# Optimization experiments

Hardware: AMD Instinct MI355X
Metric: run time of the kernel (lower is better)

## Reference

```python
import jax, jax.numpy as jnp
import numpy as np

N = 8256        # 32 graphs * 258 nodes (view in gencoder_mine requires multiple of 258)
E = 132096      # avg degree 16
D = 32          # encoding_size (in = out node feats of NNConv)
HALF = D // 2
HID = 128
NG = 32         # number of graphs
PER = 258       # hard-coded nodes per graph
OUT = 128       # out_feats
EPS = 1e-5


def _lrelu(x):
    return jnp.where(x >= 0, x, 0.2 * x)


def setup_inputs() -> dict:
    key = jax.random.key(0)
    ks = jax.random.split(key, 24)
    rn = lambda i, shape, s=0.05: jax.random.normal(ks[i], shape, dtype=jnp.float32) * s
    return {
        "pos": jax.random.normal(ks[0], (N, 3), dtype=jnp.float32),
        "vel": jax.random.normal(ks[1], (N, 3), dtype=jnp.float32),
        "edge_idx": jax.random.randint(ks[2], (2, E), 0, N),
        # node / velocity encoders: Linear(3,128) -> LeakyReLU(0.2) -> Linear(128, D/2)
        "ne_w1": rn(3, (3, HID)), "ne_b1": jnp.zeros((HID,), jnp.float32),
        "ne_w2": rn(4, (HID, HALF)), "ne_b2": jnp.zeros((HALF,), jnp.float32),
        "ve_w1": rn(5, (3, HID)), "ve_b1": jnp.zeros((HID,), jnp.float32),
        "ve_w2": rn(6, (HID, HALF)), "ve_b2": jnp.zeros((HALF,), jnp.float32),
        # edge_func: MLP(1, D*D): Lin(1,128)-ReLU-Lin(128,128)-ReLU-Lin(128,D*D) (SHARED by both conv layers)
        "em_w1": rn(7, (1, HID)), "em_b1": jnp.zeros((HID,), jnp.float32),
        "em_w2": rn(8, (HID, HID)), "em_b2": jnp.zeros((HID,), jnp.float32),
        "em_w3": rn(9, (HID, D * D), 0.02), "em_b3": jnp.zeros((D * D,), jnp.float32),
        "conv_b": jnp.zeros((D,), jnp.float32),  # shared NNConv bias
        # per-layer BatchNorm1d affine params
        "bn1_g": jnp.ones((D,), jnp.float32), "bn1_b": jnp.zeros((D,), jnp.float32),
        "bn2_g": jnp.ones((D,), jnp.float32), "bn2_b": jnp.zeros((D,), jnp.float32),
        # final LayerNorm(D)
        "ln_g": jnp.ones((D,), jnp.float32), "ln_b": jnp.zeros((D,), jnp.float32),
        # MLPbig_to_small: Lin(258*D,128)-LeakyReLU-Lin(128,OUT)
        "fc_w1": rn(10, (PER * D, HID)), "fc_b1": jnp.zeros((HID,), jnp.float32),
        "fc_w2": rn(11, (HID, OUT)), "fc_b2": jnp.zeros((OUT,), jnp.float32),
    }


def reference(pos, vel, edge_idx, ne_w1, ne_b1, ne_w2, ne_b2, ve_w1, ve_b1, ve_w2, ve_b2,
              em_w1, em_b1, em_w2, em_b2, em_w3, em_b3, conv_b,
              bn1_g, bn1_b, bn2_g, bn2_b, ln_g, ln_b, fc_w1, fc_b1, fc_w2, fc_b2):
    center = edge_idx[0]   # edge dst (messages flow neigh -> center)
    neigh = edge_idx[1]    # edge src

    # cosine-cutoff edge weight: 1/2 * (cos(dist*pi/max(dist)) + 1)
    diff = pos[center] - pos[neigh]                      # [E,3]
    dist = jnp.sqrt(jnp.sum(diff * diff, axis=1))        # [E]
    w = 0.5 * (jnp.cos(dist * jnp.pi / jnp.max(dist)) + 1.0)

    # node features: concat of pos/vel encoders -> [N, D]
    h = jnp.concatenate([
        _lrelu(pos @ ne_w1 + ne_b1) @ ne_w2 + ne_b2,
        _lrelu(vel @ ve_w1 + ve_b1) @ ve_w2 + ve_b2,
    ], axis=1)

    # per-edge NNConv weight matrices (edge MLP is shared across both conv layers)
    z = jax.nn.relu(w[:, None] @ em_w1 + em_b1)
    z = jax.nn.relu(z @ em_w2 + em_b2)
    We = (z @ em_w3 + em_b3).reshape(E, D, D)            # [E, D, D]

    deg = jax.ops.segment_sum(jnp.ones((E,), h.dtype), center, num_segments=N)
    denom = jnp.maximum(deg, 1.0)[:, None]

    # two conv layers: h = NNConv(BatchNorm(h)) + h  (shared NNConv weights)
    for g, b in ((bn1_g, bn1_b), (bn2_g, bn2_b)):
        mu = h.mean(axis=0)
        var = h.var(axis=0)  # biased, as in torch BN training mode
        hn = (h - mu) * jax.lax.rsqrt(var + EPS) * g + b
        msg = jnp.einsum('ed,edf->ef', hn[neigh], We)    # gather + per-edge matmul
        agg = jax.ops.segment_sum(msg, center, num_segments=N) / denom  # mean scatter
        h = agg + conv_b + h

    # LayerNorm over feature dim
    mu = h.mean(axis=-1, keepdims=True)
    var = h.var(axis=-1, keepdims=True)
    h = (h - mu) * jax.lax.rsqrt(var + EPS) * ln_g + ln_b

    # reshape to [NG, 258*D] and decode
    out = h.reshape(NG, PER * D)
    out = _lrelu(out @ fc_w1 + fc_b1) @ fc_w2 + fc_b2    # [NG, OUT]
    return out
```

## Files before the change

### kernel.cpp

```cpp
#include <hip/hip_runtime.h>
#include <hip/hip_bf16.h>

#define NNODE 8256
#define NEDGE 132096
#define DD 32
#define HIDN 128
#define NGR 32
#define PERG 258
#define KPG (PERG*DD)
#define NSTEP 129
#define PADE_MAX 330240
#define FC1S 86

typedef unsigned short ushortT;
typedef __attribute__((ext_vector_type(8))) short short8v;
typedef __attribute__((ext_vector_type(4))) float float4v;

__device__ __forceinline__ unsigned pk_bf16(float a, float b) {
    unsigned ua = __float_as_uint(a), ub = __float_as_uint(b);
    ua = (ua + 0x7fffu + ((ua >> 16) & 1u)) >> 16;
    ub = (ub + 0x7fffu + ((ub >> 16) & 1u)) >> 16;
    return ua | (ub << 16);
}
__device__ __forceinline__ ushortT bf16s(float a) {
    unsigned ua = __float_as_uint(a);
    return (ushortT)((ua + 0x7fffu + ((ua >> 16) & 1u)) >> 16);
}

__global__ __launch_bounds__(256) void k_encode(
    const float* __restrict__ pos, const float* __restrict__ vel,
    const float* __restrict__ nw1, const float* __restrict__ nb1,
    const float* __restrict__ nw2, const float* __restrict__ nb2,
    const float* __restrict__ vw1, const float* __restrict__ vb1,
    const float* __restrict__ vw2, const float* __restrict__ vb2,
    float* __restrict__ h)
{
    __shared__ float s_nw1[384], s_nb1[128], s_nw2[2048];
    __shared__ float s_vw1[384], s_vb1[128], s_vw2[2048];
    __shared__ float s_nb2[16], s_vb2[16];
    int t = threadIdx.x;
    for (int i = t; i < 384;  i += 256) { s_nw1[i] = nw1[i]; s_vw1[i] = vw1[i]; }
    for (int i = t; i < 128;  i += 256) { s_nb1[i] = nb1[i]; s_vb1[i] = vb1[i]; }
    for (int i = t; i < 2048; i += 256) { s_nw2[i] = nw2[i]; s_vw2[i] = vw2[i]; }
    if (t < 16) { s_nb2[t] = nb2[t]; s_vb2[t] = vb2[t]; }
    __syncthreads();

    int n = blockIdx.x * 32 + (t >> 3);
    int q = t & 7;
    float p0 = pos[n*3], p1 = pos[n*3+1], p2 = pos[n*3+2];
    float v0 = vel[n*3], v1 = vel[n*3+1], v2 = vel[n*3+2];
    float accP[16], accV[16];
    #pragma unroll
    for (int f = 0; f < 16; f++) { accP[f] = 0.f; accV[f] = 0.f; }
    int j0 = q * 16;
    #pragma unroll
    for (int jj = 0; jj < 16; jj++) {
        int j = j0 + jj;
        float hp = p0*s_nw1[j] + p1*s_nw1[128+j] + p2*s_nw1[256+j] + s_nb1[j];
        hp = hp >= 0.f ? hp : 0.2f*hp;
        float hv = v0*s_vw1[j] + v1*s_vw1[128+j] + v2*s_vw1[256+j] + s_vb1[j];
        hv = hv >= 0.f ? hv : 0.2f*hv;
        #pragma unroll
        for (int f = 0; f < 16; f++) {
            accP[f] += hp * s_nw2[j*16+f];
            accV[f] += hv * s_vw2[j*16+f];
        }
    }
    #pragma unroll
    for (int o = 1; o < 8; o <<= 1) {
        #pragma unroll
        for (int f = 0; f < 16; f++) {
            accP[f] += __shfl_xor(accP[f], o, 64);
            accV[f] += __shfl_xor(accV[f], o, 64);
        }
    }
    if (q == 0) {
        float4* op = (float4*)(h + (size_t)n*DD);
        #pragma unroll
        for (int m = 0; m < 4; m++)
            op[m] = make_float4(accP[4*m]+s_nb2[4*m], accP[4*m+1]+s_nb2[4*m+1],
                                accP[4*m+2]+s_nb2[4*m+2], accP[4*m+3]+s_nb2[4*m+3]);
        #pragma unroll
        for (int m = 0; m < 4; m++)
            op[4+m] = make_float4(accV[4*m]+s_vb2[4*m], accV[4*m+1]+s_vb2[4*m+1],
                                  accV[4*m+2]+s_vb2[4*m+2], accV[4*m+3]+s_vb2[4*m+3]);
    }
}

__global__ __launch_bounds__(256) void k_edge1(
    const float* __restrict__ pos, const int* __restrict__ ei,
    float* __restrict__ dist, unsigned* __restrict__ maxd, int* __restrict__ deg)
{
    int e = blockIdx.x * 256 + threadIdx.x;
    float dd = 0.f;
    if (e < NEDGE) {
        int c = ei[e], n = ei[NEDGE + e];
        float dx = pos[c*3]   - pos[n*3];
        float dy = pos[c*3+1] - pos[n*3+1];
        float dz = pos[c*3+2] - pos[n*3+2];
        dd = sqrtf(dx*dx + dy*dy + dz*dz);
        dist[e] = dd;
        atomicAdd(&deg[c], 1);
    }
    #pragma unroll
    for (int o = 32; o > 0; o >>= 1) dd = fmaxf(dd, __shfl_down(dd, o, 64));
    if ((threadIdx.x & 63) == 0) atomicMax(maxd, __float_as_uint(dd));
}

__global__ __launch_bounds__(1024) void k_scan(const int* __restrict__ deg, int* __restrict__ off)
{
    __shared__ int s[1024];
    int t = threadIdx.x;
    int base = t * 9;
    int loc[9]; int sum = 0;
    #pragma unroll
    for (int k = 0; k < 9; k++) {
        int i = base + k;
        int v = (i < NNODE) ? ((deg[i] + 31) & ~31) : 0;
        loc[k] = sum; sum += v;
    }
    s[t] = sum; __syncthreads();
    for (int o = 1; o < 1024; o <<= 1) {
        int v = (t >= o) ? s[t - o] : 0;
        __syncthreads();
        s[t] += v;
        __syncthreads();
    }
    int pre = (t == 0) ? 0 : s[t-1];
    #pragma unroll
    for (int k = 0; k < 9; k++) {
        int i = base + k;
        if (i < NNODE) off[i] = pre + loc[k];
    }
    if (t == 1023) off[NNODE] = s[1023];
}

__global__ __launch_bounds__(256) void k_scatter(
    const int* __restrict__ ei, const int* __restrict__ off,
    int* __restrict__ cursor, int* __restrict__ sN, int* __restrict__ sE)
{
    int e = blockIdx.x * 256 + threadIdx.x;
    if (e >= NEDGE) return;
    int c = ei[e];
    int p = off[c] + atomicAdd(&cursor[c], 1);
    sN[p] = ei[NEDGE + e];
    sE[p] = e;
}

__global__ __launch_bounds__(256) void k_packB(
    const float* __restrict__ w3, const float* __restrict__ b3, ushortT* __restrict__ Bp)
{
    int gid = blockIdx.x*256 + threadIdx.x;
    if (gid >= NSTEP*2*64) return;
    int step = gid >> 7;
    int ntile = (gid >> 6) & 1;
    int lane = gid & 63;
    int col = ntile*16 + (lane & 15);
    int kb = step*32 + 8*(lane >> 4);
    float v[8];
    #pragma unroll
    for (int j = 0; j < 8; j++) {
        int k = kb + j;
        v[j] = (k < 4096) ? w3[(size_t)k*DD + col] : b3[(size_t)(k - 4096)*DD + col];
    }
    uint4 o;
    o.x = pk_bf16(v[0], v[1]);
    o.y = pk_bf16(v[2], v[3]);
    o.z = pk_bf16(v[4], v[5]);
    o.w = pk_bf16(v[6], v[7]);
    *(uint4*)&Bp[(size_t)gid*8] = o;
}

__global__ __launch_bounds__(256) void k_packW2(
    const float* __restrict__ w2, ushortT* __restrict__ W2p)
{
    int gid = blockIdx.x*256 + threadIdx.x;
    if (gid >= 4*8*64) return;
    int s2 = gid >> 9;
    int n  = (gid >> 6) & 7;
    int lane = gid & 63;
    int col = 16*n + (lane & 15);
    int kb = 32*s2 + 8*(lane >> 4);
    float v[8];
    #pragma unroll
    for (int j = 0; j < 8; j++) v[j] = w2[(size_t)(kb + j)*HIDN + col];
    uint4 o;
    o.x = pk_bf16(v[0], v[1]);
    o.y = pk_bf16(v[2], v[3]);
    o.z = pk_bf16(v[4], v[5]);
    o.w = pk_bf16(v[6], v[7]);
    *(uint4*)&W2p[(size_t)gid*8] = o;
}

__global__ __launch_bounds__(256, 4) void k_z2(
    const float* __restrict__ dist, const unsigned* __restrict__ maxdb,
    const int* __restrict__ sE, const int* __restrict__ padOff,
    const float* __restrict__ w1, const float* __restrict__ b1,
    const ushortT* __restrict__ W2p, const float* __restrict__ b2,
    ushortT* __restrict__ z2T)
{
    int t = threadIdx.x, wv = t >> 6, ln = t & 63;
    int slotB = blockIdx.x * 64;
    int padE = padOff[NNODE];
    if (slotB >= padE) return;
    int slotW = slotB + wv*16;
    int l16 = ln & 15, lh = ln >> 4;

    float wval = -1.f;
    if (ln < 16) {
        int e = sE[slotW + ln];
        if (e >= 0) {
            float inv = 3.14159265358979323846f / __uint_as_float(*maxdb);
            wval = 0.5f * (cosf(dist[e] * inv) + 1.0f);
        }
    }

    if (wv == 0 && ln < 8) {
        uint4 u = make_uint4(0x3F803F80u, 0x3F803F80u, 0x3F803F80u, 0x3F803F80u);
        *(uint4*)&z2T[(size_t)128*PADE_MAX + (unsigned)(slotB + ln*8)] = u;
    }

    if (__ballot(ln < 16 && wval >= 0.f) == 0ull) return;

    float wrow = __shfl(wval, l16, 64);
    bool pad = (wrow < 0.f);

    float4v acc[8];
    #pragma unroll
    for (int n = 0; n < 8; n++) acc[n] = (float4v){0.f,0.f,0.f,0.f};

    #pragma unroll
    for (int s2 = 0; s2 < 4; s2++) {
        int kb = s2*32 + lh*8;
        float4 w1a = *(const float4*)&w1[kb];
        float4 w1b = *(const float4*)&w1[kb+4];
        float4 b1a = *(const float4*)&b1[kb];
        float4 b1b = *(const float4*)&b1[kb+4];
        float z0 = fmaxf(wrow*w1a.x + b1a.x, 0.f);
        float z1 = fmaxf(wrow*w1a.y + b1a.y, 0.f);
        float z2 = fmaxf(wrow*w1a.z + b1a.z, 0.f);
        float z3 = fmaxf(wrow*w1a.w + b1a.w, 0.f);
        float z4 = fmaxf(wrow*w1b.x + b1b.x, 0.f);
        float z5 = fmaxf(wrow*w1b.y + b1b.y, 0.f);
        float z6 = fmaxf(wrow*w1b.z + b1b.z, 0.f);
        float z7 = fmaxf(wrow*w1b.w + b1b.w, 0.f);
        uint4 ua;
        ua.x = pad ? 0u : pk_bf16(z0, z1);
        ua.y = pad ? 0u : pk_bf16(z2, z3);
        ua.z = pad ? 0u : pk_bf16(z4, z5);
        ua.w = pad ? 0u : pk_bf16(z6, z7);
        short8v a = *(short8v*)&ua;
        #pragma unroll
        for (int n = 0; n < 8; n++) {
            short8v b = *(const short8v*)&W2p[(size_t)((s2*8 + n)*64 + ln)*8];
            acc[n] = __builtin_amdgcn_mfma_f32_16x16x32_bf16(a, b, acc[n], 0, 0, 0);
        }
    }

    float wfl0 = __shfl(wval, 4*lh + 0, 64);
    float wfl1 = __shfl(wval, 4*lh + 1, 64);
    float wfl2 = __shfl(wval, 4*lh + 2, 64);
    float wfl3 = __shfl(wval, 4*lh + 3, 64);
    bool anyreal = (wfl0 >= 0.f) || (wfl1 >= 0.f) || (wfl2 >= 0.f) || (wfl3 >= 0.f);
    if (anyreal) {
        #pragma unroll
        for (int n = 0; n < 8; n++) {
            int col = 16*n + l16;
            float bb = b2[col];
            float v0 = (wfl0 < 0.f) ? 0.f : fmaxf(acc[n][0] + bb, 0.f);
            float v1 = (wfl1 < 0.f) ? 0.f : fmaxf(acc[n][1] + bb, 0.f);
            float v2 = (wfl2 < 0.f) ? 0.f : fmaxf(acc[n][2] + bb, 0.f);
            float v3 = (wfl3 < 0.f) ? 0.f : fmaxf(acc[n][3] + bb, 0.f);
            uint2 o = make_uint2(pk_bf16(v0, v1), pk_bf16(v2, v3));
            *(uint2*)&z2T[(size_t)col*PADE_MAX + (unsigned)(slotW + 4*lh)] = o;
        }
    }
}

__global__ __launch_bounds__(256) void k_bnstats(const float* __restrict__ h, float* __restrict__ stats)
{
    int t = threadIdx.x;
    float s = 0.f, ss = 0.f;
    for (size_t i = (size_t)blockIdx.x*256 + t; i < (size_t)NNODE*DD; i += (size_t)gridDim.x*256) {
        float v = h[i]; s += v; ss += v*v;
    }
    __shared__ float r0[256], r1[256];
    r0[t] = s; r1[t] = ss;
    __syncthreads();
    if (t < 32) {
        float a = 0.f, b = 0.f;
        for (int k = t; k < 256; k += 32) { a += r0[k]; b += r1[k]; }
        atomicAdd(&stats[t], a);
        atomicAdd(&stats[32 + t], b);
    }
}

__global__ __launch_bounds__(256) void k_hgather(
    const float* __restrict__ hn, const int* __restrict__ sN, const int* __restrict__ padOff,
    const float* __restrict__ stats,
    const float* __restrict__ bng, const float* __restrict__ bnb,
    ushortT* __restrict__ hnT)
{
    int t = threadIdx.x;
    int slotB = blockIdx.x * 128;
    if (slotB >= padOff[NNODE]) return;
    int d = t >> 3;
    int sb = slotB + (t & 7) * 16;
    float mu  = stats[d] * (1.0f/(float)NNODE);
    float var = stats[DD+d] * (1.0f/(float)NNODE) - mu*mu;
    float sc = rsqrtf(var + 1e-5f) * bng[d];
    float sh = bnb[d] - mu*sc;
    float v[16];
    #pragma unroll
    for (int i = 0; i < 16; i++) {
        int n = sN[sb + i];
        v[i] = (n >= 0) ? (hn[(size_t)n*DD + d]*sc + sh) : 0.f;
    }
    uint4 o0, o1;
    o0.x = pk_bf16(v[0], v[1]);  o0.y = pk_bf16(v[2], v[3]);
    o0.z = pk_bf16(v[4], v[5]);  o0.w = pk_bf16(v[6], v[7]);
    o1.x = pk_bf16(v[8], v[9]);  o1.y = pk_bf16(v[10], v[11]);
    o1.z = pk_bf16(v[12], v[13]);o1.w = pk_bf16(v[14], v[15]);
    *(uint4*)&hnT[(size_t)d*PADE_MAX + sb]     = o0;
    *(uint4*)&hnT[(size_t)d*PADE_MAX + sb + 8] = o1;
}

__global__ __launch_bounds__(256, 3) void k_conv(
    const float* __restrict__ hin, float* __restrict__ hout,
    const ushortT* __restrict__ z2T, const ushortT* __restrict__ hnT,
    const int* __restrict__ padOff, const int* __restrict__ deg,
    const ushortT* __restrict__ Bp, const float* __restrict__ convb)
{
    __shared__ ushortT sG[4][4128];
    __shared__ float sred[4][4][DD];

    int t = threadIdx.x, wv = t >> 6, ln = t & 63;
    int l16 = ln & 15, lh = ln >> 4;
    int c = blockIdx.x*4 + wv;
    int ks0 = padOff[c], ks1 = padOff[c+1];
    float idc = 1.f / fmaxf((float)deg[c], 1.f);

    float4v acc[9][2];
    #pragma unroll
    for (int m = 0; m < 9; m++) { acc[m][0] = (float4v){0,0,0,0}; acc[m][1] = (float4v){0,0,0,0}; }

    for (int ks = ks0; ks < ks1; ks += 32) {
        size_t kcol = (size_t)(ks + lh*8);
        short8v b0 = *(const short8v*)&hnT[(size_t)l16*PADE_MAX + kcol];
        short8v b1 = *(const short8v*)&hnT[(size_t)(16 + l16)*PADE_MAX + kcol];
        short8v a[9];
        #pragma unroll
        for (int m = 0; m < 9; m++)
            a[m] = *(const short8v*)&z2T[(size_t)(16*m + l16)*PADE_MAX + kcol];
        #pragma unroll
        for (int m = 0; m < 9; m++) {
            acc[m][0] = __builtin_amdgcn_mfma_f32_16x16x32_bf16(a[m], b0, acc[m][0], 0, 0, 0);
            acc[m][1] = __builtin_amdgcn_mfma_f32_16x16x32_bf16(a[m], b1, acc[m][1], 0, 0, 0);
        }
    }

    char* sGw = (char*)&sG[wv][0];
    #pragma unroll
    for (int m = 0; m < 9; m++) {
        #pragma unroll
        for (int r = 0; r < 4; r++) {
            int h = 16*m + 4*lh + r;
            bool live = (m < 8) || (lh == 0 && r == 0);
            if (live) {
                unsigned sw = (unsigned)(((h >> 2) & 3) << 4);
                #pragma unroll
                for (int n = 0; n < 2; n++) {
                    int d = 16*n + l16;
                    unsigned byte = (unsigned)(h*64) + (((unsigned)(d*2)) ^ sw);
                    *(ushortT*)(sGw + byte) = bf16s(acc[m][n][r] * idc);
                }
            }
        }
    }
    __syncthreads();

    float4v c0 = (float4v){0,0,0,0}, c1 = (float4v){0,0,0,0};
    for (int s = wv; s < NSTEP; s += 4) {
        short8v a = (short8v){0,0,0,0,0,0,0,0};
        if (l16 < 4) {
            unsigned sw = (unsigned)(((s >> 2) & 3) << 4);
            unsigned byte = (unsigned)(s*64) + (((unsigned)(lh*16)) ^ sw);
            a = *(const short8v*)((const char*)&sG[l16][0] + byte);
        }
        short8v b0 = *(const short8v*)&Bp[((size_t)s*2 + 0)*512 + ln*8];
        short8v b1 = *(const short8v*)&Bp[((size_t)s*2 + 1)*512 + ln*8];
        c0 = __builtin_amdgcn_mfma_f32_16x16x32_bf16(a, b0, c0, 0, 0, 0);
        c1 = __builtin_amdgcn_mfma_f32_16x16x32_bf16(a, b1, c1, 0, 0, 0);
    }
    if (lh == 0) {
        #pragma unroll
        for (int r = 0; r < 4; r++) {
            sred[wv][r][l16]      = c0[r];
            sred[wv][r][16 + l16] = c1[r];
        }
    }
    __syncthreads();

    if (t < 4*DD) {
        int cc = t >> 5, f = t & 31;
        float s = sred[0][cc][f] + sred[1][cc][f] + sred[2][cc][f] + sred[3][cc][f];
        int node = blockIdx.x*4 + cc;
        hout[(size_t)node*DD + f] = s + convb[f] + hin[(size_t)node*DD + f];
    }
}

__global__ __launch_bounds__(256) void k_ln(const float* __restrict__ h,
    const float* __restrict__ lng, const float* __restrict__ lnb, float* __restrict__ hLN)
{
    int i = blockIdx.x * 256 + threadIdx.x;
    if (i >= NNODE) return;
    const float4* hr = (const float4*)(h + (size_t)i*DD);
    float4 v[8];
    float mu = 0.f;
    #pragma unroll
    for (int q = 0; q < 8; q++) { v[q] = hr[q]; mu += v[q].x+v[q].y+v[q].z+v[q].w; }
    mu *= (1.f/32.f);
    float var = 0.f;
    #pragma unroll
    for (int q = 0; q < 8; q++) {
        float d0=v[q].x-mu, d1=v[q].y-mu, d2=v[q].z-mu, d3=v[q].w-mu;
        var += d0*d0 + d1*d1 + d2*d2 + d3*d3;
    }
    var *= (1.f/32.f);
    float rs = rsqrtf(var + 1e-5f);
    float4* o = (float4*)(hLN + (size_t)i*DD);
    #pragma unroll
    for (int q = 0; q < 8; q++) {
        float4 gq = ((const float4*)lng)[q];
        float4 bq = ((const float4*)lnb)[q];
        float4 r;
        r.x = (v[q].x-mu)*rs*gq.x + bq.x;
        r.y = (v[q].y-mu)*rs*gq.y + bq.y;
        r.z = (v[q].z-mu)*rs*gq.z + bq.z;
        r.w = (v[q].w-mu)*rs*gq.w + bq.w;
        o[q] = r;
    }
}

__global__ __launch_bounds__(256) void k_fc1(const float* __restrict__ hLN,
    const float* __restrict__ w1, float* __restrict__ partial)
{
    int g = blockIdx.x / FC1S, s = blockIdx.x % FC1S;
    int j = threadIdx.x & 127, half = threadIdx.x >> 7;
    int k0 = s*96 + half*4;
    const float* x = hLN + (size_t)g*KPG;
    float a = 0.f;
    #pragma unroll
    for (int m = 0; m < 12; m++) {
        int k = k0 + m*8;
        float4 xv = *(const float4*)&x[k];
        const float* wp = w1 + (size_t)k*HIDN + j;
        a += xv.x * wp[0];
        a += xv.y * wp[HIDN];
        a += xv.z * wp[2*HIDN];
        a += xv.w * wp[3*HIDN];
    }
    partial[((size_t)blockIdx.x*2 + half)*HIDN + j] = a;
}

__global__ __launch_bounds__(128) void k_fc2(const float* __restrict__ partial,
    const float* __restrict__ b1, const float* __restrict__ w2,
    const float* __restrict__ b2, float* __restrict__ out)
{
    __shared__ float hid[128];
    int g = blockIdx.x, t = threadIdx.x;
    float a = b1[t];
    #pragma unroll 4
    for (int p = 0; p < 2*FC1S; p++) a += partial[(size_t)(g*2*FC1S + p)*HIDN + t];
    a = a >= 0.f ? a : 0.2f*a;
    hid[t] = a;
    __syncthreads();
    float o = b2[t];
    #pragma unroll 4
    for (int j = 0; j < 128; j++) o += hid[j]*w2[j*128 + t];
    out[(size_t)g*128 + t] = o;
}

extern "C" void kernel_launch(void* const* d_in, const int* in_sizes, int n_in,
                              void* d_out, int out_size, void* d_ws, size_t ws_size,
                              hipStream_t stream)
{
    const float* pos  = (const float*)d_in[0];
    const float* vel  = (const float*)d_in[1];
    const int*   eidx = (const int*)  d_in[2];
    const float* nw1 = (const float*)d_in[3];  const float* nb1 = (const float*)d_in[4];
    const float* nw2 = (const float*)d_in[5];  const float* nb2 = (const float*)d_in[6];
    const float* vw1 = (const float*)d_in[7];  const float* vb1 = (const float*)d_in[8];
    const float* vw2 = (const float*)d_in[9];  const float* vb2 = (const float*)d_in[10];
    const float* ew1 = (const float*)d_in[11]; const float* eb1 = (const float*)d_in[12];
    const float* ew2 = (const float*)d_in[13]; const float* eb2 = (const float*)d_in[14];
    const float* ew3 = (const float*)d_in[15]; const float* eb3 = (const float*)d_in[16];
    const float* cvb = (const float*)d_in[17];
    const float* b1g = (const float*)d_in[18]; const float* b1b = (const float*)d_in[19];
    const float* b2g = (const float*)d_in[20]; const float* b2b = (const float*)d_in[21];
    const float* lng = (const float*)d_in[22]; const float* lnb = (const float*)d_in[23];
    const float* fw1 = (const float*)d_in[24]; const float* fb1 = (const float*)d_in[25];
    const float* fw2 = (const float*)d_in[26]; const float* fb2 = (const float*)d_in[27];

    char* ws = (char*)d_ws;
    size_t off = 0;
    auto alloc = [&](size_t bytes) -> void* {
        void* p = ws + off;
        off = (off + bytes + 255) & ~(size_t)255;
        return p;
    };
    unsigned* maxd  = (unsigned*)alloc(4);
    float* stats1   = (float*)alloc(64*4);
    float* stats2   = (float*)alloc(64*4);
    int* deg        = (int*)alloc((size_t)NNODE*4);
    int* cursor     = (int*)alloc((size_t)NNODE*4);
    size_t zeroBytes = off;
    int* padOff     = (int*)alloc((size_t)(NNODE+1)*4);
    int* sN         = (int*)alloc((size_t)PADE_MAX*4);
    int* sE         = (int*)alloc((size_t)PADE_MAX*4);
    float* dist     = (float*)alloc((size_t)NEDGE*4);
    float* hA       = (float*)alloc((size_t)NNODE*DD*4);
    float* hB       = (float*)alloc((size_t)NNODE*DD*4);
    float* hLN      = (float*)alloc((size_t)NNODE*DD*4);
    float* partial  = (float*)alloc((size_t)NGR*2*FC1S*HIDN*4);
    ushortT* Bp     = (ushortT*)alloc((size_t)NSTEP*2*64*8*2);
    ushortT* W2p    = (ushortT*)alloc((size_t)4*8*64*8*2);
    ushortT* z2T    = (ushortT*)alloc((size_t)129*PADE_MAX*2);
    ushortT* hnT    = (ushortT*)alloc((size_t)32*PADE_MAX*2);

    hipMemsetAsync(d_ws, 0, zeroBytes, stream);
    hipMemsetAsync(sN, 0xFF, (size_t)PADE_MAX*4, stream);
    hipMemsetAsync(sE, 0xFF, (size_t)PADE_MAX*4, stream);

    k_encode<<<NNODE/32, 256, 0, stream>>>(pos, vel, nw1, nb1, nw2, nb2,
                                           vw1, vb1, vw2, vb2, hA);
    k_edge1<<<NEDGE/256, 256, 0, stream>>>(pos, eidx, dist, maxd, deg);
    k_scan<<<1, 1024, 0, stream>>>(deg, padOff);
    k_scatter<<<NEDGE/256, 256, 0, stream>>>(eidx, padOff, cursor, sN, sE);
    k_packB<<<(NSTEP*2*64 + 255)/256, 256, 0, stream>>>(ew3, eb3, Bp);
    k_packW2<<<8, 256, 0, stream>>>(ew2, W2p);
    k_z2<<<PADE_MAX/64, 256, 0, stream>>>(dist, maxd, sE, padOff,
                                          ew1, eb1, W2p, eb2, z2T);

    k_bnstats<<<64, 256, 0, stream>>>(hA, stats1);
    k_hgather<<<PADE_MAX/128, 256, 0, stream>>>(hA, sN, padOff, stats1, b1g, b1b, hnT);
    k_conv<<<NNODE/4, 256, 0, stream>>>(hA, hB, z2T, hnT, padOff, deg, Bp, cvb);

    k_bnstats<<<64, 256, 0, stream>>>(hB, stats2);
    k_hgather<<<PADE_MAX/128, 256, 0, stream>>>(hB, sN, padOff, stats2, b2g, b2b, hnT);
    k_conv<<<NNODE/4, 256, 0, stream>>>(hB, hA, z2T, hnT, padOff, deg, Bp, cvb);

    k_ln<<<(NNODE+255)/256, 256, 0, stream>>>(hA, lng, lnb, hLN);
    k_fc1<<<NGR*FC1S, 256, 0, stream>>>(hLN, fw1, partial);
    k_fc2<<<NGR, 128, 0, stream>>>(partial, fb1, fw2, fb2, (float*)d_out);
}
```

Measured before the change: 408.9 us.

## Fuse BN stats and LayerNorm into producers, stage W2 in LDS, coalesce gather

Measured after the change: 381.6 us. -6.7%, faster.

```diff
diff --git a/kernel.cpp b/kernel.cpp
--- a/kernel.cpp
+++ b/kernel.cpp
@@ -33,11 +33,12 @@
     const float* __restrict__ nw2, const float* __restrict__ nb2,
     const float* __restrict__ vw1, const float* __restrict__ vb1,
     const float* __restrict__ vw2, const float* __restrict__ vb2,
-    float* __restrict__ h)
+    float* __restrict__ h, float* __restrict__ stats)
 {
     __shared__ float s_nw1[384], s_nb1[128], s_nw2[2048];
     __shared__ float s_vw1[384], s_vb1[128], s_vw2[2048];
     __shared__ float s_nb2[16], s_vb2[16];
+    __shared__ float s_rows[32][33];
     int t = threadIdx.x;
     for (int i = t; i < 384;  i += 256) { s_nw1[i] = nw1[i]; s_vw1[i] = vw1[i]; }
     for (int i = t; i < 128;  i += 256) { s_nb1[i] = nb1[i]; s_vb1[i] = vb1[i]; }
@@ -74,16 +75,36 @@
             accV[f] += __shfl_xor(accV[f], o, 64);
         }
     }
+    int nl = t >> 3;
     if (q == 0) {
         float4* op = (float4*)(h + (size_t)n*DD);
         #pragma unroll
-        for (int m = 0; m < 4; m++)
-            op[m] = make_float4(accP[4*m]+s_nb2[4*m], accP[4*m+1]+s_nb2[4*m+1],
-                                accP[4*m+2]+s_nb2[4*m+2], accP[4*m+3]+s_nb2[4*m+3]);
-        #pragma unroll
-        for (int m = 0; m < 4; m++)
-            op[4+m] = make_float4(accV[4*m]+s_vb2[4*m], accV[4*m+1]+s_vb2[4*m+1],
-                                  accV[4*m+2]+s_vb2[4*m+2], accV[4*m+3]+s_vb2[4*m+3]);
+        for (int m = 0; m < 4; m++) {
+            float4 r = make_float4(accP[4*m]+s_nb2[4*m], accP[4*m+1]+s_nb2[4*m+1],
+                                   accP[4*m+2]+s_nb2[4*m+2], accP[4*m+3]+s_nb2[4*m+3]);
+            op[m] = r;
+            s_rows[nl][4*m+0] = r.x; s_rows[nl][4*m+1] = r.y;
+            s_rows[nl][4*m+2] = r.z; s_rows[nl][4*m+3] = r.w;
+        }
+        #pragma unroll
+        for (int m = 0; m < 4; m++) {
+            float4 r = make_float4(accV[4*m]+s_vb2[4*m], accV[4*m+1]+s_vb2[4*m+1],
+                                   accV[4*m+2]+s_vb2[4*m+2], accV[4*m+3]+s_vb2[4*m+3]);
+            op[4+m] = r;
+            s_rows[nl][16+4*m+0] = r.x; s_rows[nl][16+4*m+1] = r.y;
+            s_rows[nl][16+4*m+2] = r.z; s_rows[nl][16+4*m+3] = r.w;
+        }
+    }
+    __syncthreads();
+    if (t < 32) {
+        float s = 0.f, ss = 0.f;
+        #pragma unroll 8
+        for (int r = 0; r < 32; r++) {
+            float v = s_rows[r][t];
+            s += v; ss += v*v;
+        }
+        atomicAdd(&stats[t], s);
+        atomicAdd(&stats[32 + t], ss);
     }
 }
 
@@ -199,10 +220,20 @@
     const ushortT* __restrict__ W2p, const float* __restrict__ b2,
     ushortT* __restrict__ z2T)
 {
+    __shared__ __align__(16) ushortT sW2[16384];
     int t = threadIdx.x, wv = t >> 6, ln = t & 63;
     int slotB = blockIdx.x * 64;
     int padE = padOff[NNODE];
     if (slotB >= padE) return;
+
+    {
+        const uint4* src = (const uint4*)W2p;
+        uint4* dst = (uint4*)sW2;
+        #pragma unroll
+        for (int i = 0; i < 8; i++) dst[t + i*256] = src[t + i*256];
+    }
+    __syncthreads();
+
     int slotW = slotB + wv*16;
     int l16 = ln & 15, lh = ln >> 4;
 
@@ -252,7 +283,7 @@
         short8v a = *(short8v*)&ua;
         #pragma unroll
         for (int n = 0; n < 8; n++) {
-            short8v b = *(const short8v*)&W2p[(size_t)((s2*8 + n)*64 + ln)*8];
+            short8v b = *(const short8v*)&sW2[(size_t)((s2*8 + n)*64 + ln)*8];
             acc[n] = __builtin_amdgcn_mfma_f32_16x16x32_bf16(a, b, acc[n], 0, 0, 0);
         }
     }
@@ -277,65 +308,72 @@
     }
 }
 
-__global__ __launch_bounds__(256) void k_bnstats(const float* __restrict__ h, float* __restrict__ stats)
-{
-    int t = threadIdx.x;
-    float s = 0.f, ss = 0.f;
-    for (size_t i = (size_t)blockIdx.x*256 + t; i < (size_t)NNODE*DD; i += (size_t)gridDim.x*256) {
-        float v = h[i]; s += v; ss += v*v;
-    }
-    __shared__ float r0[256], r1[256];
-    r0[t] = s; r1[t] = ss;
-    __syncthreads();
-    if (t < 32) {
-        float a = 0.f, b = 0.f;
-        for (int k = t; k < 256; k += 32) { a += r0[k]; b += r1[k]; }
-        atomicAdd(&stats[t], a);
-        atomicAdd(&stats[32 + t], b);
-    }
-}
-
 __global__ __launch_bounds__(256) void k_hgather(
     const float* __restrict__ hn, const int* __restrict__ sN, const int* __restrict__ padOff,
     const float* __restrict__ stats,
     const float* __restrict__ bng, const float* __restrict__ bnb,
     ushortT* __restrict__ hnT)
 {
+    __shared__ float s_scale[DD], s_shift[DD];
+    __shared__ ushortT sT[DD][66];
     int t = threadIdx.x;
-    int slotB = blockIdx.x * 128;
+    if (t < DD) {
+        float mu  = stats[t] * (1.0f/(float)NNODE);
+        float var = stats[DD+t] * (1.0f/(float)NNODE) - mu*mu;
+        float sc = rsqrtf(var + 1e-5f) * bng[t];
+        s_scale[t] = sc;
+        s_shift[t] = bnb[t] - mu*sc;
+    }
+    __syncthreads();
+    int slotB = blockIdx.x * 64;
     if (slotB >= padOff[NNODE]) return;
-    int d = t >> 3;
-    int sb = slotB + (t & 7) * 16;
-    float mu  = stats[d] * (1.0f/(float)NNODE);
-    float var = stats[DD+d] * (1.0f/(float)NNODE) - mu*mu;
-    float sc = rsqrtf(var + 1e-5f) * bng[d];
-    float sh = bnb[d] - mu*sc;
-    float v[16];
-    #pragma unroll
-    for (int i = 0; i < 16; i++) {
-        int n = sN[sb + i];
-        v[i] = (n >= 0) ? (hn[(size_t)n*DD + d]*sc + sh) : 0.f;
-    }
-    uint4 o0, o1;
-    o0.x = pk_bf16(v[0], v[1]);  o0.y = pk_bf16(v[2], v[3]);
-    o0.z = pk_bf16(v[4], v[5]);  o0.w = pk_bf16(v[6], v[7]);
-    o1.x = pk_bf16(v[8], v[9]);  o1.y = pk_bf16(v[10], v[11]);
-    o1.z = pk_bf16(v[12], v[13]);o1.w = pk_bf16(v[14], v[15]);
-    *(uint4*)&hnT[(size_t)d*PADE_MAX + sb]     = o0;
-    *(uint4*)&hnT[(size_t)d*PADE_MAX + sb + 8] = o1;
+    int sl = t >> 2, q = t & 3;
+    int n = sN[slotB + sl];
+    float v[8];
+    if (n >= 0) {
+        const float* hr = hn + (size_t)n*DD + q*8;
+        float4 x0 = *(const float4*)hr;
+        float4 x1 = *(const float4*)(hr + 4);
+        int c0 = q*8;
+        v[0] = x0.x*s_scale[c0+0] + s_shift[c0+0];
+        v[1] = x0.y*s_scale[c0+1] + s_shift[c0+1];
+        v[2] = x0.z*s_scale[c0+2] + s_shift[c0+2];
+        v[3] = x0.w*s_scale[c0+3] + s_shift[c0+3];
+        v[4] = x1.x*s_scale[c0+4] + s_shift[c0+4];
+        v[5] = x1.y*s_scale[c0+5] + s_shift[c0+5];
+        v[6] = x1.z*s_scale[c0+6] + s_shift[c0+6];
+        v[7] = x1.w*s_scale[c0+7] + s_shift[c0+7];
+    } else {
+        #pragma unroll
+        for (int j = 0; j < 8; j++) v[j] = 0.f;
+    }
+    #pragma unroll
+    for (int j = 0; j < 8; j++) sT[q*8 + j][sl] = bf16s(v[j]);
+    __syncthreads();
+    int d = t >> 3, p = t & 7;
+    unsigned w0 = (unsigned)sT[d][p*8+0] | ((unsigned)sT[d][p*8+1] << 16);
+    unsigned w1 = (unsigned)sT[d][p*8+2] | ((unsigned)sT[d][p*8+3] << 16);
+    unsigned w2 = (unsigned)sT[d][p*8+4] | ((unsigned)sT[d][p*8+5] << 16);
+    unsigned w3 = (unsigned)sT[d][p*8+6] | ((unsigned)sT[d][p*8+7] << 16);
+    *(uint4*)&hnT[(size_t)d*PADE_MAX + slotB + p*8] = make_uint4(w0, w1, w2, w3);
 }
 
 __global__ __launch_bounds__(256, 3) void k_conv(
     const float* __restrict__ hin, float* __restrict__ hout,
     const ushortT* __restrict__ z2T, const ushortT* __restrict__ hnT,
     const int* __restrict__ padOff, const int* __restrict__ deg,
-    const ushortT* __restrict__ Bp, const float* __restrict__ convb)
+    const ushortT* __restrict__ Bp, const float* __restrict__ convb,
+    float* __restrict__ statsOut,
+    const float* __restrict__ lng, const float* __restrict__ lnb,
+    float* __restrict__ hLNout)
 {
     __shared__ ushortT sG[4][4128];
     __shared__ float sred[4][4][DD];
+    __shared__ float s_stat[64];
 
     int t = threadIdx.x, wv = t >> 6, ln = t & 63;
     int l16 = ln & 15, lh = ln >> 4;
+    if (t < 64) s_stat[t] = 0.f;
     int c = blockIdx.x*4 + wv;
     int ks0 = padOff[c], ks1 = padOff[c+1];
     float idc = 1.f / fmaxf((float)deg[c], 1.f);
@@ -379,19 +417,36 @@
     }
     __syncthreads();
 
+    const char* sGb = (const char*)&sG[l16 & 3][0];
     float4v c0 = (float4v){0,0,0,0}, c1 = (float4v){0,0,0,0};
-    for (int s = wv; s < NSTEP; s += 4) {
-        short8v a = (short8v){0,0,0,0,0,0,0,0};
-        if (l16 < 4) {
-            unsigned sw = (unsigned)(((s >> 2) & 3) << 4);
-            unsigned byte = (unsigned)(s*64) + (((unsigned)(lh*16)) ^ sw);
-            a = *(const short8v*)((const char*)&sG[l16][0] + byte);
-        }
-        short8v b0 = *(const short8v*)&Bp[((size_t)s*2 + 0)*512 + ln*8];
-        short8v b1 = *(const short8v*)&Bp[((size_t)s*2 + 1)*512 + ln*8];
-        c0 = __builtin_amdgcn_mfma_f32_16x16x32_bf16(a, b0, c0, 0, 0, 0);
-        c1 = __builtin_amdgcn_mfma_f32_16x16x32_bf16(a, b1, c1, 0, 0, 0);
-    }
+    float4v d0 = (float4v){0,0,0,0}, d1 = (float4v){0,0,0,0};
+    int s = wv;
+    for (; s + 4 < NSTEP; s += 8) {
+        int s2 = s + 4;
+        unsigned byA = (unsigned)(s*64)  + (((unsigned)(lh*16)) ^ (unsigned)(((s  >> 2) & 3) << 4));
+        unsigned byB = (unsigned)(s2*64) + (((unsigned)(lh*16)) ^ (unsigned)(((s2 >> 2) & 3) << 4));
+        short8v aA = *(const short8v*)(sGb + byA);
+        short8v aB = *(const short8v*)(sGb + byB);
+        short8v b0A = *(const short8v*)&Bp[((size_t)s*2  + 0)*512 + ln*8];
+        short8v b1A = *(const short8v*)&Bp[((size_t)s*2  + 1)*512 + ln*8];
+        short8v b0B = *(const short8v*)&Bp[((size_t)s2*2 + 0)*512 + ln*8];
+        short8v b1B = *(const short8v*)&Bp[((size_t)s2*2 + 1)*512 + ln*8];
+        c0 = __builtin_amdgcn_mfma_f32_16x16x32_bf16(aA, b0A, c0, 0, 0, 0);
+        c1 = __builtin_amdgcn_mfma_f32_16x16x32_bf16(aA, b1A, c1, 0, 0, 0);
+        d0 = __builtin_amdgcn_mfma_f32_16x16x32_bf16(aB, b0B, d0, 0, 0, 0);
+        d1 = __builtin_amdgcn_mfma_f32_16x16x32_bf16(aB, b1B, d1, 0, 0, 0);
+    }
+    for (; s < NSTEP; s += 4) {
+        unsigned byA = (unsigned)(s*64) + (((unsigned)(lh*16)) ^ (unsigned)(((s >> 2) & 3) << 4));
+        short8v aA = *(const short8v*)(sGb + byA);
+        short8v b0A = *(const short8v*)&Bp[((size_t)s*2 + 0)*512 + ln*8];
+        short8v b1A = *(const short8v*)&Bp[((size_t)s*2 + 1)*512 + ln*8];
+        c0 = __builtin_amdgcn_mfma_f32_16x16x32_bf16(aA, b0A, c0, 0, 0, 0);
+        c1 = __builtin_amdgcn_mfma_f32_16x16x32_bf16(aA, b1A, c1, 0, 0, 0);
+    }
+    #pragma unroll
+    for (int r = 0; r < 4; r++) { c0[r] += d0[r]; c1[r] += d1[r]; }
+
     if (lh == 0) {
         #pragma unroll
         for (int r = 0; r < 4; r++) {
@@ -403,42 +458,30 @@
 
     if (t < 4*DD) {
         int cc = t >> 5, f = t & 31;
-        float s = sred[0][cc][f] + sred[1][cc][f] + sred[2][cc][f] + sred[3][cc][f];
+        float sv = sred[0][cc][f] + sred[1][cc][f] + sred[2][cc][f] + sred[3][cc][f];
         int node = blockIdx.x*4 + cc;
-        hout[(size_t)node*DD + f] = s + convb[f] + hin[(size_t)node*DD + f];
-    }
-}
-
-__global__ __launch_bounds__(256) void k_ln(const float* __restrict__ h,
-    const float* __restrict__ lng, const float* __restrict__ lnb, float* __restrict__ hLN)
-{
-    int i = blockIdx.x * 256 + threadIdx.x;
-    if (i >= NNODE) return;
-    const float4* hr = (const float4*)(h + (size_t)i*DD);
-    float4 v[8];
-    float mu = 0.f;
-    #pragma unroll
-    for (int q = 0; q < 8; q++) { v[q] = hr[q]; mu += v[q].x+v[q].y+v[q].z+v[q].w; }
-    mu *= (1.f/32.f);
-    float var = 0.f;
-    #pragma unroll
-    for (int q = 0; q < 8; q++) {
-        float d0=v[q].x-mu, d1=v[q].y-mu, d2=v[q].z-mu, d3=v[q].w-mu;
-        var += d0*d0 + d1*d1 + d2*d2 + d3*d3;
-    }
-    var *= (1.f/32.f);
-    float rs = rsqrtf(var + 1e-5f);
-    float4* o = (float4*)(hLN + (size_t)i*DD);
-    #pragma unroll
-    for (int q = 0; q < 8; q++) {
-        float4 gq = ((const float4*)lng)[q];
-        float4 bq = ((const float4*)lnb)[q];
-        float4 r;
-        r.x = (v[q].x-mu)*rs*gq.x + bq.x;
-        r.y = (v[q].y-mu)*rs*gq.y + bq.y;
-        r.z = (v[q].z-mu)*rs*gq.z + bq.z;
-        r.w = (v[q].w-mu)*rs*gq.w + bq.w;
-        o[q] = r;
+        sv += convb[f] + hin[(size_t)node*DD + f];
+        hout[(size_t)node*DD + f] = sv;
+        if (statsOut) {
+            atomicAdd(&s_stat[f], sv);
+            atomicAdd(&s_stat[32 + f], sv*sv);
+        }
+        if (hLNout) {
+            float m1 = sv, m2 = sv*sv;
+            #pragma unroll
+            for (int o = 1; o < 32; o <<= 1) {
+                m1 += __shfl_xor(m1, o, 32);
+                m2 += __shfl_xor(m2, o, 32);
+            }
+            m1 *= (1.f/32.f);
+            float var = m2*(1.f/32.f) - m1*m1;
+            float rs = rsqrtf(var + 1e-5f);
+            hLNout[(size_t)node*DD + f] = (sv - m1)*rs*lng[f] + lnb[f];
+        }
+    }
+    if (statsOut) {
+        __syncthreads();
+        if (t < 64) atomicAdd(&statsOut[t], s_stat[t]);
     }
 }
 
@@ -533,7 +576,7 @@
     hipMemsetAsync(sE, 0xFF, (size_t)PADE_MAX*4, stream);
 
     k_encode<<<NNODE/32, 256, 0, stream>>>(pos, vel, nw1, nb1, nw2, nb2,
-                                           vw1, vb1, vw2, vb2, hA);
+                                           vw1, vb1, vw2, vb2, hA, stats1);
     k_edge1<<<NEDGE/256, 256, 0, stream>>>(pos, eidx, dist, maxd, deg);
     k_scan<<<1, 1024, 0, stream>>>(deg, padOff);
     k_scatter<<<NEDGE/256, 256, 0, stream>>>(eidx, padOff, cursor, sN, sE);
@@ -542,15 +585,14 @@
     k_z2<<<PADE_MAX/64, 256, 0, stream>>>(dist, maxd, sE, padOff,
                                           ew1, eb1, W2p, eb2, z2T);
 
-    k_bnstats<<<64, 256, 0, stream>>>(hA, stats1);
-    k_hgather<<<PADE_MAX/128, 256, 0, stream>>>(hA, sN, padOff, stats1, b1g, b1b, hnT);
-    k_conv<<<NNODE/4, 256, 0, stream>>>(hA, hB, z2T, hnT, padOff, deg, Bp, cvb);
-
-    k_bnstats<<<64, 256, 0, stream>>>(hB, stats2);
-    k_hgather<<<PADE_MAX/128, 256, 0, stream>>>(hB, sN, padOff, stats2, b2g, b2b, hnT);
-    k_conv<<<NNODE/4, 256, 0, stream>>>(hB, hA, z2T, hnT, padOff, deg, Bp, cvb);
-
-    k_ln<<<(NNODE+255)/256, 256, 0, stream>>>(hA, lng, lnb, hLN);
+    k_hgather<<<PADE_MAX/64, 256, 0, stream>>>(hA, sN, padOff, stats1, b1g, b1b, hnT);
+    k_conv<<<NNODE/4, 256, 0, stream>>>(hA, hB, z2T, hnT, padOff, deg, Bp, cvb,
+                                        stats2, nullptr, nullptr, nullptr);
+
+    k_hgather<<<PADE_MAX/64, 256, 0, stream>>>(hB, sN, padOff, stats2, b2g, b2b, hnT);
+    k_conv<<<NNODE/4, 256, 0, stream>>>(hB, hA, z2T, hnT, padOff, deg, Bp, cvb,
+                                        nullptr, lng, lnb, hLN);
+
     k_fc1<<<NGR*FC1S, 256, 0, stream>>>(hLN, fw1, partial);
     k_fc2<<<NGR, 128, 0, stream>>>(partial, fb1, fw2, fb2, (float*)d_out);
 }
```
